# Performance work log

Measured on AMD Instinct MI355X. Metric: run time of the kernel, lower is better.

The kernel has to match this reference:

```python
import jax, jax.numpy as jnp
import numpy as np

OUT_H = 7
OUT_W = 7
SPATIAL_SCALE = 0.25
SAMPLING_RATIO = 2  # exact sampling branch (sampling_ratio > 0)
ALIGNED = True


def setup_inputs() -> dict:
    key = jax.random.key(0)
    k1, k2, k3, k4 = jax.random.split(key, 4)
    feat = jax.random.normal(k1, (4, 256, 100, 100), dtype=jnp.float32)
    # rois[K,5]: (batch_idx, x1, y1, x2, y2) in image coords (image ~400px since scale=0.25)
    K = 512
    bidx = jax.random.randint(k2, (K,), 0, 4).astype(jnp.float32)
    xy1 = jax.random.uniform(k3, (K, 2), minval=0.0, maxval=300.0, dtype=jnp.float32)
    wh = jax.random.uniform(k4, (K, 2), minval=20.0, maxval=99.0, dtype=jnp.float32)
    xy2 = xy1 + wh
    rois = jnp.concatenate([bidx[:, None], xy1[:, 0:1], xy1[:, 1:2], xy2[:, 0:1], xy2[:, 1:2]], axis=1)
    return {"input": feat, "rois": rois}


def _roi_align(feat, rois):
    N, C, H, W = feat.shape
    b = rois[:, 0].astype(jnp.int32)  # [K]
    offset = 0.5 if ALIGNED else 0.0
    sw = rois[:, 1] * SPATIAL_SCALE - offset
    sh = rois[:, 2] * SPATIAL_SCALE - offset
    ew = rois[:, 3] * SPATIAL_SCALE - offset
    eh = rois[:, 4] * SPATIAL_SCALE - offset
    rw = ew - sw
    rh = eh - sh
    if not ALIGNED:
        rw = jnp.maximum(rw, 1.0)
        rh = jnp.maximum(rh, 1.0)
    bin_h = rh / OUT_H  # [K]
    bin_w = rw / OUT_W

    ph = jnp.arange(OUT_H, dtype=feat.dtype)
    pw = jnp.arange(OUT_W, dtype=feat.dtype)
    samp = jnp.arange(SAMPLING_RATIO, dtype=feat.dtype) + 0.5  # (i + 0.5)

    # y: [K, OUT_H, SR], x: [K, OUT_W, SR]
    y = sh[:, None, None] + ph[None, :, None] * bin_h[:, None, None] + samp[None, None, :] * (bin_h / SAMPLING_RATIO)[:, None, None]
    x = sw[:, None, None] + pw[None, :, None] * bin_w[:, None, None] + samp[None, None, :] * (bin_w / SAMPLING_RATIO)[:, None, None]

    # bilinear interpolation indices/weights (matches _bilinear_interpolate)
    y = jnp.maximum(y, 0.0)
    x = jnp.maximum(x, 0.0)
    yl = y.astype(jnp.int32)
    xl = x.astype(jnp.int32)
    yh = jnp.where(yl >= H - 1, H - 1, yl + 1)
    yl = jnp.where(yl >= H - 1, H - 1, yl)
    xh = jnp.where(xl >= W - 1, W - 1, xl + 1)
    xl = jnp.where(xl >= W - 1, W - 1, xl)
    ly = y - yl.astype(feat.dtype)
    lx = x - xl.astype(feat.dtype)
    hy = 1.0 - ly
    hx = 1.0 - lx

    def gather(yi, xi):
        # yi: [K,PH,IY], xi: [K,PW,IX] -> [K,PH,IY,PW,IX,C]
        return feat[b[:, None, None, None, None], :,
                    yi[:, :, :, None, None],
                    xi[:, None, None, :, :]]

    v1 = gather(yl, xl)
    v2 = gather(yl, xh)
    v3 = gather(yh, xl)
    v4 = gather(yh, xh)

    out = (jnp.einsum('kpi,kqj,kpiqjc->kcpq', hy, hx, v1)
           + jnp.einsum('kpi,kqj,kpiqjc->kcpq', hy, lx, v2)
           + jnp.einsum('kpi,kqj,kpiqjc->kcpq', ly, hx, v3)
           + jnp.einsum('kpi,kqj,kpiqjc->kcpq', ly, lx, v4))
    count = float(max(SAMPLING_RATIO * SAMPLING_RATIO, 1))
    return out / count  # [K, C, OUT_H, OUT_W]


def reference(input, rois):
    return _roi_align(input, rois)
```

## Files before the change

kernel.cpp:

```cpp
#include <hip/hip_runtime.h>


#define FEAT_C 256
#define FEAT_H 100
#define FEAT_W 100
#define HW     10000
#define NROI   512
#define NBINS  49
#define IMG_N  4

#define REC_BYTES  32
#define IMG_STRIDE (NROI * NBINS * REC_BYTES)
#define CNT_OFF    (IMG_N * IMG_STRIDE)

typedef float f32x2 __attribute__((ext_vector_type(2)));

__device__ __forceinline__ void samp_geo(float s, float bsz, int idx, int sr_i,
                                         int& lo, float& fr) {
    float v = s + bsz * ((float)idx + ((float)sr_i + 0.5f) * 0.5f);
    v = fmaxf(v, 0.0f);
    int l = (int)v;
    if (l > FEAT_H - 1) l = FEAT_H - 1;
    fr = v - (float)l;
    lo = l;
}

__global__ __launch_bounds__(64) void roialign_setup(
    const float* __restrict__ rois, char* __restrict__ ws)
{
    const int k    = blockIdx.x;
    const int lane = threadIdx.x;
    const float* r = rois + k * 5;
    const int bk   = (int)r[0];

    int slot = 0, total = 0;
    for (int i = 0; i < NROI; i += 64) {
        int bi = (int)rois[(i + lane) * 5];
        unsigned long long m = __ballot(bi == bk);
        total += __popcll(m);
        int rel = k - i;
        unsigned long long lt = rel <= 0 ? 0ull
                              : (rel >= 64 ? ~0ull : ((1ull << rel) - 1ull));
        slot += __popcll(m & lt);
    }
    if (lane == 0) ((int*)(ws + CNT_OFF))[bk] = total;

    if (lane < NBINS) {
        const float sw = r[1] * 0.25f - 0.5f, sh = r[2] * 0.25f - 0.5f;
        const float ew = r[3] * 0.25f - 0.5f, eh = r[4] * 0.25f - 0.5f;
        const float bh = (eh - sh) * (1.0f / 7.0f);
        const float bw = (ew - sw) * (1.0f / 7.0f);
        const int ph = (lane * 37) >> 8;
        const int pw = lane - ph * 7;
        int ylA, ylB, xl0, xl1; float lyA, lyB, lx0, lx1;
        samp_geo(sh, bh, ph, 0, ylA, lyA);
        samp_geo(sh, bh, ph, 1, ylB, lyB);
        samp_geo(sw, bw, pw, 0, xl0, lx0);
        samp_geo(sw, bw, pw, 1, xl1, lx1);
        if (xl0 >= FEAT_W - 1) lx0 = 0.0f;
        if (xl1 >= FEAT_W - 1) lx1 = 0.0f;
        int yhA = min(ylA + 1, FEAT_H - 1), yhB = min(ylB + 1, FEAT_H - 1);
        uint4 a, b2;
        a.x  = (unsigned)(ylA * 400) | ((unsigned)(yhA * 400) << 16);
        a.y  = (unsigned)(ylB * 400) | ((unsigned)(yhB * 400) << 16);
        a.z  = (unsigned)(xl0 * 4)   | ((unsigned)(xl1 * 4)   << 16);
        a.w  = __float_as_uint(lyA);
        b2.x = __float_as_uint(lyB);
        b2.y = __float_as_uint(lx0);
        b2.z = __float_as_uint(lx1);
        b2.w = (unsigned)(k * (FEAT_C * NBINS) + lane);
        char* dst = ws + bk * IMG_STRIDE + (slot * NBINS + lane) * REC_BYTES;
        *(uint4*)dst        = a;
        *(uint4*)(dst + 16) = b2;
    }
}

__global__ __launch_bounds__(512, 4) void roialign_main(
    const float* __restrict__ feat, const char* __restrict__ ws,
    float* __restrict__ out)
{
    __shared__ __align__(16) float s_img[2 * HW + 8];

    const int bid = blockIdx.x;
    const int img = bid & 3;
    const int cp  = bid >> 2;
    const int tid = threadIdx.x;

    const float* c0 = feat + (size_t)(img * FEAT_C + 2 * cp) * HW;
    const float* c1 = c0 + HW;
    for (int t = tid; t < HW / 4; t += 512) {
        float4 A = ((const float4*)c0)[t];
        float4 B = ((const float4*)c1)[t];
        ((float4*)s_img)[2 * t]     = make_float4(A.x, B.x, A.y, B.y);
        ((float4*)s_img)[2 * t + 1] = make_float4(A.z, B.z, A.w, B.w);
    }
    if (tid < 8) s_img[2 * HW + tid] = 0.0f;

    int cnt = ((const int*)(ws + CNT_OFF))[img];
    const int nrec = (cnt < 0 || cnt > NROI) ? 0 : cnt * NBINS;
    const char* rb = ws + img * IMG_STRIDE;
    float* const oc = out + (size_t)(2 * cp) * NBINS;

    int   idx = tid;
    uint4 ra, rk;
    if (idx < nrec) {
        const char* p = rb + (size_t)idx * REC_BYTES;
        ra = *(const uint4*)p;
        rk = *(const uint4*)(p + 16);
    }
    __syncthreads();

    while (idx < nrec) {
        const uint4 a = ra, b2 = rk;
        const int nidx = idx + 512;
        if (nidx < nrec) {
            const char* p = rb + (size_t)nidx * REC_BYTES;
            ra = *(const uint4*)p;
            rk = *(const uint4*)(p + 16);
        }

        const char* base = (const char*)s_img;
        const int oAl = (a.x & 0xffff) * 2, oAh = (a.x >> 16) * 2;
        const int oBl = (a.y & 0xffff) * 2, oBh = (a.y >> 16) * 2;
        const int x0  = (a.z & 0xffff) * 2, x1  = (a.z >> 16) * 2;
        const float lyA = __uint_as_float(a.w),  hyA = 1.0f - lyA;
        const float lyB = __uint_as_float(rk.x == rk.x ? b2.x : b2.x), hyB = 1.0f - __uint_as_float(b2.x);
        const float lx0 = __uint_as_float(b2.y), hx0 = 1.0f - lx0;
        const float lx1 = __uint_as_float(b2.z), hx1 = 1.0f - lx1;

        const f32x2* pAl0 = (const f32x2*)(base + oAl + x0);
        const f32x2* pAl1 = (const f32x2*)(base + oAl + x1);
        const f32x2* pAh0 = (const f32x2*)(base + oAh + x0);
        const f32x2* pAh1 = (const f32x2*)(base + oAh + x1);
        const f32x2* pBl0 = (const f32x2*)(base + oBl + x0);
        const f32x2* pBl1 = (const f32x2*)(base + oBl + x1);
        const f32x2* pBh0 = (const f32x2*)(base + oBh + x0);
        const f32x2* pBh1 = (const f32x2*)(base + oBh + x1);

        f32x2 sAl = pAl0[0] * hx0 + pAl0[1] * lx0 + pAl1[0] * hx1 + pAl1[1] * lx1;
        f32x2 sAh = pAh0[0] * hx0 + pAh0[1] * lx0 + pAh1[0] * hx1 + pAh1[1] * lx1;
        f32x2 sBl = pBl0[0] * hx0 + pBl0[1] * lx0 + pBl1[0] * hx1 + pBl1[1] * lx1;
        f32x2 sBh = pBh0[0] * hx0 + pBh0[1] * lx0 + pBh1[0] * hx1 + pBh1[1] * lx1;
        f32x2 acc = (sAl * hyA + sAh * lyA + sBl * hyB + sBh * __uint_as_float(b2.x)) * 0.25f;

        float* o = oc + b2.w;
        o[0]     = acc.x;
        o[NBINS] = acc.y;
        idx = nidx;
    }
}

extern "C" void kernel_launch(void* const* d_in, const int* in_sizes, int n_in,
                              void* d_out, int out_size, void* d_ws, size_t ws_size,
                              hipStream_t stream) {
    const float* feat = (const float*)d_in[0];
    const float* rois = (const float*)d_in[1];
    float*       outp = (float*)d_out;
    roialign_setup<<<dim3(NROI), dim3(64), 0, stream>>>(rois, (char*)d_ws);
    roialign_main<<<dim3(IMG_N * (FEAT_C / 2)), dim3(512), 0, stream>>>(
        feat, (const char*)d_ws, outp);
}
```

Baseline: 100.6 us.

## Process four channels per block with register-prefetched second plane and padded rows

Each block now runs 1024 threads over four channels as two channel-pair passes. The feature data for the second pair is loaded into registers while the first pass runs, then written to a second shared buffer. Rows are padded to 102 pairs so the edge sample reads an explicit zero instead of the next row. This hides part of the global load latency and halves the block count, at the cost of 160 KB of shared memory per block (limiting residency to one block per CU), more register pressure, and an extra barrier.

```diff
diff --git a/kernel.cpp b/kernel.cpp
--- a/kernel.cpp
+++ b/kernel.cpp
@@ -12,6 +12,9 @@
 #define REC_BYTES  32
 #define IMG_STRIDE (NROI * NBINS * REC_BYTES)
 #define CNT_OFF    (IMG_N * IMG_STRIDE)
+
+#define ROWP   102
+#define PLANEP (ROWP * FEAT_H)
 
 typedef float f32x2 __attribute__((ext_vector_type(2)));
 
@@ -61,8 +64,8 @@
         if (xl1 >= FEAT_W - 1) lx1 = 0.0f;
         int yhA = min(ylA + 1, FEAT_H - 1), yhB = min(ylB + 1, FEAT_H - 1);
         uint4 a, b2;
-        a.x  = (unsigned)(ylA * 400) | ((unsigned)(yhA * 400) << 16);
-        a.y  = (unsigned)(ylB * 400) | ((unsigned)(yhB * 400) << 16);
+        a.x  = (unsigned)(ylA * ROWP) | ((unsigned)(yhA * ROWP) << 16);
+        a.y  = (unsigned)(ylB * ROWP) | ((unsigned)(yhB * ROWP) << 16);
         a.z  = (unsigned)(xl0 * 4)   | ((unsigned)(xl1 * 4)   << 16);
         a.w  = __float_as_uint(lyA);
         b2.x = __float_as_uint(lyB);
@@ -75,79 +78,107 @@
     }
 }
 
-__global__ __launch_bounds__(512, 4) void roialign_main(
+__device__ __forceinline__ void wr_pairs(f32x2* buf, int t, float4 A, float4 B) {
+    const int r = (t * 1311) >> 15;
+    const int p = ROWP * r + 4 * (t - 25 * r);
+    float4* d = (float4*)&buf[p];
+    d[0] = make_float4(A.x, B.x, A.y, B.y);
+    d[1] = make_float4(A.z, B.z, A.w, B.w);
+}
+
+__global__ __launch_bounds__(1024, 4) void roialign_main(
     const float* __restrict__ feat, const char* __restrict__ ws,
     float* __restrict__ out)
 {
-    __shared__ __align__(16) float s_img[2 * HW + 8];
+    __shared__ __align__(16) f32x2 s_buf[2][PLANEP];
 
     const int bid = blockIdx.x;
     const int img = bid & 3;
-    const int cp  = bid >> 2;
+    const int q   = bid >> 2;
     const int tid = threadIdx.x;
 
-    const float* c0 = feat + (size_t)(img * FEAT_C + 2 * cp) * HW;
+    const float* c0 = feat + (size_t)(img * FEAT_C + 4 * q) * HW;
     const float* c1 = c0 + HW;
-    for (int t = tid; t < HW / 4; t += 512) {
+
+    for (int t = tid; t < HW / 4; t += 1024) {
         float4 A = ((const float4*)c0)[t];
         float4 B = ((const float4*)c1)[t];
-        ((float4*)s_img)[2 * t]     = make_float4(A.x, B.x, A.y, B.y);
-        ((float4*)s_img)[2 * t + 1] = make_float4(A.z, B.z, A.w, B.w);
+        wr_pairs(s_buf[0], t, A, B);
     }
-    if (tid < 8) s_img[2 * HW + tid] = 0.0f;
+    if (tid < FEAT_H) {
+        s_buf[0][ROWP * tid + FEAT_W] = f32x2{0.0f, 0.0f};
+        s_buf[1][ROWP * tid + FEAT_W] = f32x2{0.0f, 0.0f};
+    }
 
     int cnt = ((const int*)(ws + CNT_OFF))[img];
     const int nrec = (cnt < 0 || cnt > NROI) ? 0 : cnt * NBINS;
     const char* rb = ws + img * IMG_STRIDE;
-    float* const oc = out + (size_t)(2 * cp) * NBINS;
 
-    int   idx = tid;
-    uint4 ra, rk;
-    if (idx < nrec) {
-        const char* p = rb + (size_t)idx * REC_BYTES;
-        ra = *(const uint4*)p;
-        rk = *(const uint4*)(p + 16);
-    }
-    __syncthreads();
+    const float4* c2v = (const float4*)(c0 + 2 * HW);
+    const float4* c3v = (const float4*)(c0 + 3 * HW);
+    const int t1 = tid + 1024, t2 = tid + 2048;
+    float4 sa0 = c2v[tid], sb0 = c3v[tid];
+    float4 sa1 = c2v[t1],  sb1 = c3v[t1];
+    float4 sa2, sb2;
+    if (t2 < HW / 4) { sa2 = c2v[t2]; sb2 = c3v[t2]; }
 
-    while (idx < nrec) {
-        const uint4 a = ra, b2 = rk;
-        const int nidx = idx + 512;
-        if (nidx < nrec) {
-            const char* p = rb + (size_t)nidx * REC_BYTES;
+    auto rec_loop = [&](const f32x2* sbase, float* ocp) {
+        int   idx = tid;
+        uint4 ra, rk;
+        if (idx < nrec) {
+            const char* p = rb + (size_t)idx * REC_BYTES;
             ra = *(const uint4*)p;
             rk = *(const uint4*)(p + 16);
         }
+        __syncthreads();
 
-        const char* base = (const char*)s_img;
-        const int oAl = (a.x & 0xffff) * 2, oAh = (a.x >> 16) * 2;
-        const int oBl = (a.y & 0xffff) * 2, oBh = (a.y >> 16) * 2;
-        const int x0  = (a.z & 0xffff) * 2, x1  = (a.z >> 16) * 2;
-        const float lyA = __uint_as_float(a.w),  hyA = 1.0f - lyA;
-        const float lyB = __uint_as_float(rk.x == rk.x ? b2.x : b2.x), hyB = 1.0f - __uint_as_float(b2.x);
-        const float lx0 = __uint_as_float(b2.y), hx0 = 1.0f - lx0;
-        const float lx1 = __uint_as_float(b2.z), hx1 = 1.0f - lx1;
+        while (idx < nrec) {
+            const uint4 a = ra, b = rk;
+            const int nidx = idx + 1024;
+            if (nidx < nrec) {
+                const char* p = rb + (size_t)nidx * REC_BYTES;
+                ra = *(const uint4*)p;
+                rk = *(const uint4*)(p + 16);
+            }
 
-        const f32x2* pAl0 = (const f32x2*)(base + oAl + x0);
-        const f32x2* pAl1 = (const f32x2*)(base + oAl + x1);
-        const f32x2* pAh0 = (const f32x2*)(base + oAh + x0);
-        const f32x2* pAh1 = (const f32x2*)(base + oAh + x1);
-        const f32x2* pBl0 = (const f32x2*)(base + oBl + x0);
-        const f32x2* pBl1 = (const f32x2*)(base + oBl + x1);
-        const f32x2* pBh0 = (const f32x2*)(base + oBh + x0);
-        const f32x2* pBh1 = (const f32x2*)(base + oBh + x1);
+            const char* base = (const char*)sbase;
+            const int oAl = (a.x & 0xffff) * 8, oAh = (a.x >> 16) * 8;
+            const int oBl = (a.y & 0xffff) * 8, oBh = (a.y >> 16) * 8;
+            const int x0  = (a.z & 0xffff) * 2, x1  = (a.z >> 16) * 2;
+            const float lyA = __uint_as_float(a.w), hyA = 1.0f - lyA;
+            const float lyB = __uint_as_float(b.x), hyB = 1.0f - lyB;
+            const float lx0 = __uint_as_float(b.y), hx0 = 1.0f - lx0;
+            const float lx1 = __uint_as_float(b.z), hx1 = 1.0f - lx1;
 
-        f32x2 sAl = pAl0[0] * hx0 + pAl0[1] * lx0 + pAl1[0] * hx1 + pAl1[1] * lx1;
-        f32x2 sAh = pAh0[0] * hx0 + pAh0[1] * lx0 + pAh1[0] * hx1 + pAh1[1] * lx1;
-        f32x2 sBl = pBl0[0] * hx0 + pBl0[1] * lx0 + pBl1[0] * hx1 + pBl1[1] * lx1;
-        f32x2 sBh = pBh0[0] * hx0 + pBh0[1] * lx0 + pBh1[0] * hx1 + pBh1[1] * lx1;
-        f32x2 acc = (sAl * hyA + sAh * lyA + sBl * hyB + sBh * __uint_as_float(b2.x)) * 0.25f;
+            const f32x2* pAl0 = (const f32x2*)(base + oAl + x0);
+            const f32x2* pAl1 = (const f32x2*)(base + oAl + x1);
+            const f32x2* pAh0 = (const f32x2*)(base + oAh + x0);
+            const f32x2* pAh1 = (const f32x2*)(base + oAh + x1);
+            const f32x2* pBl0 = (const f32x2*)(base + oBl + x0);
+            const f32x2* pBl1 = (const f32x2*)(base + oBl + x1);
+            const f32x2* pBh0 = (const f32x2*)(base + oBh + x0);
+            const f32x2* pBh1 = (const f32x2*)(base + oBh + x1);
 
-        float* o = oc + b2.w;
-        o[0]     = acc.x;
-        o[NBINS] = acc.y;
-        idx = nidx;
-    }
+            f32x2 sAl = pAl0[0] * hx0 + pAl0[1] * lx0 + pAl1[0] * hx1 + pAl1[1] * lx1;
+            f32x2 sAh = pAh0[0] * hx0 + pAh0[1] * lx0 + pAh1[0] * hx1 + pAh1[1] * lx1;
+            f32x2 sBl = pBl0[0] * hx0 + pBl0[1] * lx0 + pBl1[0] * hx1 + pBl1[1] * lx1;
+            f32x2 sBh = pBh0[0] * hx0 + pBh0[1] * lx0 + pBh1[0] * hx1 + pBh1[1] * lx1;
+            f32x2 acc = (sAl * hyA + sAh * lyA + sBl * hyB + sBh * lyB) * 0.25f;
+
+            float* o = ocp + b.w;
+            o[0]     = acc.x;
+            o[NBINS] = acc.y;
+            idx = nidx;
+        }
+    };
+
+    rec_loop(s_buf[0], out + (size_t)(4 * q) * NBINS);
+
+    wr_pairs(s_buf[1], tid, sa0, sb0);
+    wr_pairs(s_buf[1], t1,  sa1, sb1);
+    if (t2 < HW / 4) wr_pairs(s_buf[1], t2, sa2, sb2);
+
+    rec_loop(s_buf[1], out + (size_t)(4 * q + 2) * NBINS);
 }
 
 extern "C" void kernel_launch(void* const* d_in, const int* in_sizes, int n_in,
@@ -157,6 +188,6 @@
     const float* rois = (const float*)d_in[1];
     float*       outp = (float*)d_out;
     roialign_setup<<<dim3(NROI), dim3(64), 0, stream>>>(rois, (char*)d_ws);
-    roialign_main<<<dim3(IMG_N * (FEAT_C / 2)), dim3(512), 0, stream>>>(
+    roialign_main<<<dim3(IMG_N * (FEAT_C / 4)), dim3(1024), 0, stream>>>(
         feat, (const char*)d_ws, outp);
 }
```

Measured after the change: 101.6 us. About the same (+1.0%).
